# Kernel tuning notes

Measured on AMD Instinct MI355X. Metric: run time of the kernel, lower is better.

## Reference

```python
import jax, jax.numpy as jnp
import numpy as np

B, D_IN, H1, H2, LAT, K = 32768, 512, 256, 128, 64, 2048
BN_EPS = 1e-5
COMMIT = 0.25


def _linear_w(k, i, o):
    # xavier-uniform-ish init
    lim = np.sqrt(6.0 / (i + o)).astype(np.float32)
    return jax.random.uniform(k, (i, o), jnp.float32, -lim, lim)


def _bn_params(keys, n):
    g = jax.random.uniform(keys[0], (n,), jnp.float32, 0.5, 1.5)
    b = 0.1 * jax.random.normal(keys[1], (n,), jnp.float32)
    m = 0.1 * jax.random.normal(keys[2], (n,), jnp.float32)
    v = jax.random.uniform(keys[3], (n,), jnp.float32, 0.5, 1.5)
    return g, b, m, v


def setup_inputs() -> dict:
    key = jax.random.key(0)
    ks = jax.random.split(key, 32)
    inp = {"x": jax.random.normal(ks[0], (B, D_IN), jnp.float32)}
    # encoder: 512 -> 256 -> 128 -> 64
    inp["ew1"], inp["eb1"] = _linear_w(ks[1], D_IN, H1), jnp.zeros((H1,), jnp.float32)
    inp["eg1"], inp["ebt1"], inp["em1"], inp["ev1"] = _bn_params(jax.random.split(ks[2], 4), H1)
    inp["ew2"], inp["eb2"] = _linear_w(ks[3], H1, H2), jnp.zeros((H2,), jnp.float32)
    inp["eg2"], inp["ebt2"], inp["em2"], inp["ev2"] = _bn_params(jax.random.split(ks[4], 4), H2)
    inp["ew3"], inp["eb3"] = _linear_w(ks[5], H2, LAT), jnp.zeros((LAT,), jnp.float32)
    # codebook (num_embeddings, latent_dim)
    inp["codebook"] = _linear_w(ks[6], K, LAT).reshape(K, LAT)
    # decoder: 64 -> 128 -> 256 -> 512
    inp["dw1"], inp["db1"] = _linear_w(ks[7], LAT, H2), jnp.zeros((H2,), jnp.float32)
    inp["dg1"], inp["dbt1"], inp["dm1"], inp["dv1"] = _bn_params(jax.random.split(ks[8], 4), H2)
    inp["dw2"], inp["db2"] = _linear_w(ks[9], H2, H1), jnp.zeros((H1,), jnp.float32)
    inp["dg2"], inp["dbt2"], inp["dm2"], inp["dv2"] = _bn_params(jax.random.split(ks[10], 4), H1)
    inp["dw3"], inp["db3"] = _linear_w(ks[11], H1, D_IN), jnp.zeros((D_IN,), jnp.float32)
    return inp


def _bn(x, g, b, m, v):
    # BatchNorm1d in eval mode: running stats
    return (x - m) * (g * jax.lax.rsqrt(v + BN_EPS)) + b


def reference(x, ew1, eb1, eg1, ebt1, em1, ev1,
              ew2, eb2, eg2, ebt2, em2, ev2,
              ew3, eb3, codebook,
              dw1, db1, dg1, dbt1, dm1, dv1,
              dw2, db2, dg2, dbt2, dm2, dv2,
              dw3, db3):
    # ---- encoder MLP (Dropout is identity in eval) ----
    h = _bn(jax.nn.relu(x @ ew1 + eb1), eg1, ebt1, em1, ev1)
    h = _bn(jax.nn.relu(h @ ew2 + eb2), eg2, ebt2, em2, ev2)
    z_e = h @ ew3 + eb3  # [B, LAT]

    # ---- vector quantization: cdist + argmin + gather ----
    # squared L2 distance (argmin-equivalent to cdist p=2)
    d2 = (jnp.sum(z_e * z_e, axis=1, keepdims=True)
          + jnp.sum(codebook * codebook, axis=1)[None, :]
          - 2.0 * (z_e @ codebook.T))  # [B, K]
    idx = jnp.argmin(d2, axis=-1)  # [B]
    z_q = codebook[idx]  # gather, [B, LAT]

    codebook_loss = jnp.mean((z_q - jax.lax.stop_gradient(z_e)) ** 2)
    commit_loss = jnp.mean((z_e - jax.lax.stop_gradient(z_q)) ** 2)
    vq_loss = codebook_loss + COMMIT * commit_loss

    # straight-through estimator
    z_q = z_e + jax.lax.stop_gradient(z_q - z_e)

    # ---- decoder MLP ----
    h = _bn(jax.nn.relu(z_q @ dw1 + db1), dg1, dbt1, dm1, dv1)
    h = _bn(jax.nn.relu(h @ dw2 + db2), dg2, dbt2, dm2, dv2)
    x_recon = h @ dw3 + db3  # [B, D_IN]

    recon_err = jnp.mean((x_recon - x) ** 2)
    return x_recon, vq_loss, idx, recon_err
```

## Files before the change

### kernel.cpp

```cpp
#include <hip/hip_runtime.h>

#define B_ROWS 32768
#define D_IN   512
#define H1_N   256
#define H2_N   128
#define LAT_N  64
#define K_CB   2048

#define BM 128
#define BN 128
#define BK 32

#define VQ_MARGIN 4.0e-3f

typedef __attribute__((ext_vector_type(8))) short s8v;
typedef __attribute__((ext_vector_type(4))) float f4v;

__device__ inline unsigned short f2bf(float f) {
    union { float f; unsigned u; } v; v.f = f;
    unsigned r = v.u + 0x7fffu + ((v.u >> 16) & 1u);
    return (unsigned short)(r >> 16);
}
__device__ inline float bf2f(unsigned short h) {
    union { unsigned u; float f; } v; v.u = ((unsigned)h) << 16;
    return v.f;
}

#define SWZ(row) ((((row) >> 2) & 7) << 3)

template <int MODE>
__global__ __launch_bounds__(256, 2) void gemm_fused(
    const float* __restrict__ A, const float* __restrict__ W,
    const float* __restrict__ bias,
    const float* __restrict__ bn_g, const float* __restrict__ bn_b,
    const float* __restrict__ bn_m, const float* __restrict__ bn_v,
    float* __restrict__ out,
    const float* __restrict__ xref, float* __restrict__ partials,
    int M, int N)
{
    __shared__ float sA[BK][BM];
    __shared__ float sB[BK][BN];
    const int tid = threadIdx.x;
    const int tr = tid >> 4;
    const int tc = tid & 15;
    const int row0 = blockIdx.x * BM;
    const int n0   = blockIdx.y * BN;

    float acc[8][8];
#pragma unroll
    for (int i = 0; i < 8; ++i)
#pragma unroll
        for (int j = 0; j < 8; ++j) acc[i][j] = 0.f;

    for (int k0 = 0; k0 < M; k0 += BK) {
#pragma unroll
        for (int it = 0; it < 4; ++it) {
            int s = tid + it * 256;
            int m = s >> 3;
            int kq = s & 7;
            float4 v = *reinterpret_cast<const float4*>(
                &A[(size_t)(row0 + m) * M + k0 + kq * 4]);
            int kk = kq * 4;
            sA[kk + 0][m ^ SWZ(kk + 0)] = v.x;
            sA[kk + 1][m ^ SWZ(kk + 1)] = v.y;
            sA[kk + 2][m ^ SWZ(kk + 2)] = v.z;
            sA[kk + 3][m ^ SWZ(kk + 3)] = v.w;
        }
#pragma unroll
        for (int it = 0; it < 4; ++it) {
            int s = tid + it * 256;
            int k = s >> 5;
            int nq = s & 31;
            int n = n0 + nq * 4;
            float4 v = make_float4(0.f, 0.f, 0.f, 0.f);
            if (n < N)
                v = *reinterpret_cast<const float4*>(&W[(size_t)(k0 + k) * N + n]);
            *reinterpret_cast<float4*>(&sB[k][nq * 4]) = v;
        }
        __syncthreads();
#pragma unroll 4
        for (int k = 0; k < BK; ++k) {
            int ac = (tr * 8) ^ SWZ(k);
            float4 a0 = *reinterpret_cast<float4*>(&sA[k][ac]);
            float4 a1 = *reinterpret_cast<float4*>(&sA[k][ac + 4]);
            float4 b0 = *reinterpret_cast<float4*>(&sB[k][tc * 8]);
            float4 b1 = *reinterpret_cast<float4*>(&sB[k][tc * 8 + 4]);
            float a[8] = {a0.x, a0.y, a0.z, a0.w, a1.x, a1.y, a1.z, a1.w};
            float b[8] = {b0.x, b0.y, b0.z, b0.w, b1.x, b1.y, b1.z, b1.w};
#pragma unroll
            for (int i = 0; i < 8; ++i)
#pragma unroll
                for (int j = 0; j < 8; ++j)
                    acc[i][j] = fmaf(a[i], b[j], acc[i][j]);
        }
        __syncthreads();
    }

    const int nb = n0 + tc * 8;
    float sq = 0.f;
    if (nb < N) {
        float bi[8], sc[8], sh[8];
#pragma unroll
        for (int j = 0; j < 8; ++j) {
            int n = nb + j;
            bi[j] = bias[n];
            if (MODE == 0) {
                float s = bn_g[n] * rsqrtf(bn_v[n] + 1e-5f);
                sc[j] = s;
                sh[j] = bn_b[n] - bn_m[n] * s;
            }
        }
#pragma unroll
        for (int i = 0; i < 8; ++i) {
            int row = row0 + tr * 8 + i;
            float o[8];
#pragma unroll
            for (int j = 0; j < 8; ++j) {
                float v = acc[i][j] + bi[j];
                if (MODE == 0) {
                    v = v > 0.f ? v : 0.f;
                    v = v * sc[j] + sh[j];
                }
                o[j] = v;
            }
            if (MODE == 2) {
#pragma unroll
                for (int j = 0; j < 8; ++j) {
                    float d = o[j] - xref[(size_t)row * N + nb + j];
                    sq = fmaf(d, d, sq);
                }
            }
            *reinterpret_cast<float4*>(&out[(size_t)row * N + nb]) =
                make_float4(o[0], o[1], o[2], o[3]);
            *reinterpret_cast<float4*>(&out[(size_t)row * N + nb + 4]) =
                make_float4(o[4], o[5], o[6], o[7]);
        }
    }
    if (MODE == 2) {
        __syncthreads();
        float* red = &sA[0][0];
        red[tid] = sq;
        __syncthreads();
        for (int off = 128; off > 0; off >>= 1) {
            if (tid < off) red[tid] += red[tid + off];
            __syncthreads();
        }
        if (tid == 0) partials[blockIdx.y * gridDim.x + blockIdx.x] = red[0];
    }
}

__global__ __launch_bounds__(256) void vq_prep(
    const float* __restrict__ cb, unsigned short* __restrict__ cb_hi,
    unsigned short* __restrict__ cb_lo, float* __restrict__ cn,
    int* __restrict__ rcnt)
{
    if (blockIdx.x == 0 && threadIdx.x == 0) rcnt[0] = 0;
    int j = blockIdx.x * 256 + threadIdx.x;
    float s = 0.f;
#pragma unroll
    for (int lq = 0; lq < 16; ++lq) {
        float4 v = *reinterpret_cast<const float4*>(&cb[(size_t)j * LAT_N + lq * 4]);
        float e[4] = {v.x, v.y, v.z, v.w};
        ushort4 h, l;
        unsigned short* hp = &h.x;
        unsigned short* lp = &l.x;
#pragma unroll
        for (int t = 0; t < 4; ++t) {
            s = fmaf(e[t], e[t], s);
            unsigned short hb = f2bf(e[t]);
            hp[t] = hb;
            lp[t] = f2bf(e[t] - bf2f(hb));
        }
        *reinterpret_cast<ushort4*>(&cb_hi[(size_t)j * LAT_N + lq * 4]) = h;
        *reinterpret_cast<ushort4*>(&cb_lo[(size_t)j * LAT_N + lq * 4]) = l;
    }
    cn[j] = s;
}

__global__ __launch_bounds__(256) void vq_mfma(
    const float* __restrict__ z, const unsigned short* __restrict__ cb_hi,
    const unsigned short* __restrict__ cb_lo, const float* __restrict__ cnorm,
    float4* __restrict__ cand)
{
    const int lane = threadIdx.x & 63;
    const int wid  = blockIdx.x * 4 + (threadIdx.x >> 6);
    const int rbase = (wid >> 3) * 64;
    const int cblk  = wid & 7;
    const int cbase = cblk * 256;
    const int lr = lane & 15;
    const int lg = lane >> 4;

    s8v a_hi[4][2], a_lo[4][2];
#pragma unroll
    for (int rt = 0; rt < 4; ++rt) {
        int row = rbase + rt * 16 + lr;
#pragma unroll
        for (int ks = 0; ks < 2; ++ks) {
            const float* p = &z[(size_t)row * LAT_N + ks * 32 + lg * 8];
            float4 v0 = *reinterpret_cast<const float4*>(p);
            float4 v1 = *reinterpret_cast<const float4*>(p + 4);
            float vv[8] = {v0.x, v0.y, v0.z, v0.w, v1.x, v1.y, v1.z, v1.w};
#pragma unroll
            for (int jj = 0; jj < 8; ++jj) {
                unsigned short hb = f2bf(vv[jj]);
                a_hi[rt][ks][jj] = (short)hb;
                a_lo[rt][ks][jj] = (short)f2bf(vv[jj] - bf2f(hb));
            }
        }
    }

    float b1[4][4], b2[4][4];
    int j1[4][4];
#pragma unroll
    for (int rt = 0; rt < 4; ++rt)
#pragma unroll
        for (int i = 0; i < 4; ++i) {
            b1[rt][i] = 3.4e38f; b2[rt][i] = 3.4e38f; j1[rt][i] = 0;
        }

    for (int ct = 0; ct < 16; ++ct) {
        int col = cbase + ct * 16 + lr;
        const unsigned short* ph = &cb_hi[(size_t)col * LAT_N + lg * 8];
        const unsigned short* pl = &cb_lo[(size_t)col * LAT_N + lg * 8];
        s8v bh0 = *reinterpret_cast<const s8v*>(ph);
        s8v bh1 = *reinterpret_cast<const s8v*>(ph + 32);
        s8v bl0 = *reinterpret_cast<const s8v*>(pl);
        s8v bl1 = *reinterpret_cast<const s8v*>(pl + 32);
        float cn = cnorm[col];
#pragma unroll
        for (int rt = 0; rt < 4; ++rt) {
            f4v acc = {0.f, 0.f, 0.f, 0.f};
            acc = __builtin_amdgcn_mfma_f32_16x16x32_bf16(a_hi[rt][0], bh0, acc, 0, 0, 0);
            acc = __builtin_amdgcn_mfma_f32_16x16x32_bf16(a_hi[rt][1], bh1, acc, 0, 0, 0);
            acc = __builtin_amdgcn_mfma_f32_16x16x32_bf16(a_lo[rt][0], bh0, acc, 0, 0, 0);
            acc = __builtin_amdgcn_mfma_f32_16x16x32_bf16(a_lo[rt][1], bh1, acc, 0, 0, 0);
            acc = __builtin_amdgcn_mfma_f32_16x16x32_bf16(a_hi[rt][0], bl0, acc, 0, 0, 0);
            acc = __builtin_amdgcn_mfma_f32_16x16x32_bf16(a_hi[rt][1], bl1, acc, 0, 0, 0);
#pragma unroll
            for (int i = 0; i < 4; ++i) {
                float d = fmaf(-2.f, acc[i], cn);
                if (d < b1[rt][i]) {
                    b2[rt][i] = b1[rt][i];
                    b1[rt][i] = d;
                    j1[rt][i] = col;
                } else if (d < b2[rt][i]) {
                    b2[rt][i] = d;
                }
            }
        }
    }

#pragma unroll
    for (int off = 1; off < 16; off <<= 1) {
#pragma unroll
        for (int rt = 0; rt < 4; ++rt)
#pragma unroll
            for (int i = 0; i < 4; ++i) {
                float o1 = __shfl_xor(b1[rt][i], off);
                float o2 = __shfl_xor(b2[rt][i], off);
                int oj = __shfl_xor(j1[rt][i], off);
                float nb2 = fminf(fmaxf(b1[rt][i], o1), fminf(b2[rt][i], o2));
                if (o1 < b1[rt][i] ||
                    (o1 == b1[rt][i] && oj < j1[rt][i])) {
                    b1[rt][i] = o1;
                    j1[rt][i] = oj;
                }
                b2[rt][i] = nb2;
            }
    }
    if (lr == 0) {
#pragma unroll
        for (int rt = 0; rt < 4; ++rt)
#pragma unroll
            for (int i = 0; i < 4; ++i) {
                int row = rbase + rt * 16 + lg * 4 + i;
                cand[(size_t)row * 8 + cblk] = make_float4(
                    b1[rt][i], __int_as_float(j1[rt][i]), b2[rt][i], 0.f);
            }
    }
}

__global__ __launch_bounds__(256) void vq_merge(
    const float4* __restrict__ cand, float* __restrict__ idxf,
    int* __restrict__ rlist, int* __restrict__ rcnt)
{
    int row = blockIdx.x * 256 + threadIdx.x;
    const float4* c = &cand[(size_t)row * 8];
    float4 c0 = c[0];
    float b1 = c0.x, b2 = c0.z;
    int j1 = __float_as_int(c0.y);
#pragma unroll
    for (int t = 1; t < 8; ++t) {
        float4 ct = c[t];
        float o1 = ct.x, o2 = ct.z;
        int oj = __float_as_int(ct.y);
        float nb2 = fminf(fmaxf(b1, o1), fminf(b2, o2));
        if (o1 < b1 || (o1 == b1 && oj < j1)) { b1 = o1; j1 = oj; }
        b2 = nb2;
    }
    idxf[row] = (float)j1;
    if (!(b2 - b1 >= VQ_MARGIN)) {
        int s = atomicAdd(rcnt, 1);
        if (s < B_ROWS) rlist[s] = row;
    }
}

#define RB 8
__global__ __launch_bounds__(256) void vq_repair(
    const int* __restrict__ rcnt, const int* __restrict__ rlist,
    const float* __restrict__ z, const float* __restrict__ cb,
    const float* __restrict__ cn, float* __restrict__ idxf)
{
    __shared__ float sz[RB][LAT_N];
    __shared__ float rv[256];
    __shared__ int ri[256];
    const int tid = threadIdx.x;
    const int count = min(rcnt[0], B_ROWS);
    for (int base = blockIdx.x * RB; base < count; base += gridDim.x * RB) {
        int nr = min(RB, count - base);
        __syncthreads();
        for (int s = tid; s < nr * LAT_N; s += 256) {
            int r = s >> 6, d = s & 63;
            int rr = rlist[base + r];
            rr = ((unsigned)rr < (unsigned)B_ROWS) ? rr : 0;
            sz[r][d] = z[(size_t)rr * LAT_N + d];
        }
        __syncthreads();
        float bv[RB];
        int bj[RB];
#pragma unroll
        for (int r = 0; r < RB; ++r) { bv[r] = 3.4e38f; bj[r] = 0; }
        for (int k = 0; k < K_CB / 256; ++k) {
            int cidx = tid + k * 256;
            float acc[RB];
#pragma unroll
            for (int r = 0; r < RB; ++r) acc[r] = 0.f;
            const float* cp = &cb[(size_t)cidx * LAT_N];
#pragma unroll
            for (int d4 = 0; d4 < 16; ++d4) {
                float4 cv = *reinterpret_cast<const float4*>(cp + d4 * 4);
#pragma unroll
                for (int r = 0; r < RB; ++r) {
                    acc[r] = fmaf(sz[r][d4 * 4 + 0], cv.x, acc[r]);
                    acc[r] = fmaf(sz[r][d4 * 4 + 1], cv.y, acc[r]);
                    acc[r] = fmaf(sz[r][d4 * 4 + 2], cv.z, acc[r]);
                    acc[r] = fmaf(sz[r][d4 * 4 + 3], cv.w, acc[r]);
                }
            }
            float cnv = cn[cidx];
#pragma unroll
            for (int r = 0; r < RB; ++r) {
                float d = fmaf(-2.f, acc[r], cnv);
                if (d < bv[r] || (d == bv[r] && cidx < bj[r])) {
                    bv[r] = d; bj[r] = cidx;
                }
            }
        }
        for (int r = 0; r < RB; ++r) {
            if (r >= nr) break;
            rv[tid] = bv[r];
            ri[tid] = bj[r];
            __syncthreads();
            for (int off = 128; off > 0; off >>= 1) {
                if (tid < off) {
                    float ov = rv[tid + off];
                    int oi = ri[tid + off];
                    if (ov < rv[tid] || (ov == rv[tid] && oi < ri[tid])) {
                        rv[tid] = ov; ri[tid] = oi;
                    }
                }
                __syncthreads();
            }
            if (tid == 0) {
                int rr = rlist[base + r];
                if ((unsigned)rr < (unsigned)B_ROWS)
                    idxf[rr] = (float)ri[0];
            }
            __syncthreads();
        }
    }
}

__global__ __launch_bounds__(256) void vq_zqloss(
    const float* __restrict__ idxf, const float* __restrict__ z,
    const float* __restrict__ cb, float* __restrict__ zq,
    float* __restrict__ partials)
{
    __shared__ float red[256];
    int tid = threadIdx.x;
    int row = blockIdx.x * 256 + tid;
    int bj = (int)idxf[row];
    bj = ((unsigned)bj < (unsigned)K_CB) ? bj : 0;
    float sq = 0.f;
#pragma unroll
    for (int lq = 0; lq < 16; ++lq) {
        float4 cv = *reinterpret_cast<const float4*>(&cb[(size_t)bj * LAT_N + lq * 4]);
        float4 zv = *reinterpret_cast<const float4*>(&z[(size_t)row * LAT_N + lq * 4]);
        *reinterpret_cast<float4*>(&zq[(size_t)row * LAT_N + lq * 4]) = cv;
        float d0 = cv.x - zv.x, d1 = cv.y - zv.y;
        float d2 = cv.z - zv.z, d3 = cv.w - zv.w;
        sq = fmaf(d0, d0, sq); sq = fmaf(d1, d1, sq);
        sq = fmaf(d2, d2, sq); sq = fmaf(d3, d3, sq);
    }
    red[tid] = sq;
    __syncthreads();
    for (int off = 128; off > 0; off >>= 1) {
        if (tid < off) red[tid] += red[tid + off];
        __syncthreads();
    }
    if (tid == 0) partials[blockIdx.x] = red[0];
}

__global__ __launch_bounds__(256) void finalize_kernel(
    const float* __restrict__ vqp, int nvq,
    const float* __restrict__ rep, int nre,
    float* __restrict__ vq_out, float* __restrict__ re_out)
{
    __shared__ float s[256];
    int tid = threadIdx.x;
    float a = 0.f;
    for (int i = tid; i < nvq; i += 256) a += vqp[i];
    s[tid] = a;
    __syncthreads();
    for (int off = 128; off > 0; off >>= 1) {
        if (tid < off) s[tid] += s[tid + off];
        __syncthreads();
    }
    if (tid == 0) *vq_out = 1.25f * s[0] / (float)(B_ROWS * LAT_N);
    __syncthreads();
    float b = 0.f;
    for (int i = tid; i < nre; i += 256) b += rep[i];
    s[tid] = b;
    __syncthreads();
    for (int off = 128; off > 0; off >>= 1) {
        if (tid < off) s[tid] += s[tid + off];
        __syncthreads();
    }
    if (tid == 0) *re_out = s[0] / (float)(B_ROWS * D_IN);
}

extern "C" void kernel_launch(void* const* d_in, const int* in_sizes, int n_in,
                              void* d_out, int out_size, void* d_ws, size_t ws_size,
                              hipStream_t stream)
{
    const float* x    = (const float*)d_in[0];
    const float* ew1  = (const float*)d_in[1];
    const float* eb1  = (const float*)d_in[2];
    const float* eg1  = (const float*)d_in[3];
    const float* ebt1 = (const float*)d_in[4];
    const float* em1  = (const float*)d_in[5];
    const float* ev1  = (const float*)d_in[6];
    const float* ew2  = (const float*)d_in[7];
    const float* eb2  = (const float*)d_in[8];
    const float* eg2  = (const float*)d_in[9];
    const float* ebt2 = (const float*)d_in[10];
    const float* em2  = (const float*)d_in[11];
    const float* ev2  = (const float*)d_in[12];
    const float* ew3  = (const float*)d_in[13];
    const float* eb3  = (const float*)d_in[14];
    const float* cb   = (const float*)d_in[15];
    const float* dw1  = (const float*)d_in[16];
    const float* db1  = (const float*)d_in[17];
    const float* dg1  = (const float*)d_in[18];
    const float* dbt1 = (const float*)d_in[19];
    const float* dm1  = (const float*)d_in[20];
    const float* dv1  = (const float*)d_in[21];
    const float* dw2  = (const float*)d_in[22];
    const float* db2  = (const float*)d_in[23];
    const float* dg2  = (const float*)d_in[24];
    const float* dbt2 = (const float*)d_in[25];
    const float* dm2  = (const float*)d_in[26];
    const float* dv2  = (const float*)d_in[27];
    const float* dw3  = (const float*)d_in[28];
    const float* db3  = (const float*)d_in[29];

    float* outf = (float*)d_out;
    const size_t XR_OFF = 0;
    const size_t VQ_OFF = (size_t)B_ROWS * D_IN;
    const size_t IDX_OFF = VQ_OFF + 1;
    const size_t RE_OFF = IDX_OFF + B_ROWS;

    float* wsf = (float*)d_ws;
    size_t off = 0;
    float* buf256 = wsf + off; off += (size_t)B_ROWS * H1_N;
    float* buf128 = wsf + off; off += (size_t)B_ROWS * H2_N;
    float* zbuf   = wsf + off; off += (size_t)B_ROWS * LAT_N;
    float* zqbuf  = wsf + off; off += (size_t)B_ROWS * LAT_N;
    float* cnbuf  = wsf + off; off += K_CB;
    float* vqp    = wsf + off; off += 128;
    float* rep    = wsf + off; off += 1024;
    unsigned short* cbhi = (unsigned short*)(wsf + off); off += K_CB * LAT_N / 2;
    unsigned short* cblo = (unsigned short*)(wsf + off); off += K_CB * LAT_N / 2;
    float4* candb = (float4*)(wsf + off); off += (size_t)B_ROWS * 8 * 4;
    int* rcnt  = (int*)(wsf + off); off += 16;
    int* rlist = (int*)(wsf + off); off += B_ROWS;

    dim3 blk(256);
    const int GX = B_ROWS / BM;

    vq_prep<<<dim3(K_CB / 256), blk, 0, stream>>>(cb, cbhi, cblo, cnbuf, rcnt);

    gemm_fused<0><<<dim3(GX, H1_N / BN), blk, 0, stream>>>(
        x, ew1, eb1, eg1, ebt1, em1, ev1, buf256, nullptr, nullptr, D_IN, H1_N);
    gemm_fused<0><<<dim3(GX, 1), blk, 0, stream>>>(
        buf256, ew2, eb2, eg2, ebt2, em2, ev2, buf128, nullptr, nullptr, H1_N, H2_N);
    gemm_fused<1><<<dim3(GX, 1), blk, 0, stream>>>(
        buf128, ew3, eb3, nullptr, nullptr, nullptr, nullptr, zbuf, nullptr, nullptr,
        H2_N, LAT_N);

    vq_mfma<<<dim3(1024), blk, 0, stream>>>(zbuf, cbhi, cblo, cnbuf, candb);
    vq_merge<<<dim3(B_ROWS / 256), blk, 0, stream>>>(
        candb, outf + IDX_OFF, rlist, rcnt);
    vq_repair<<<dim3(128), blk, 0, stream>>>(
        rcnt, rlist, zbuf, cb, cnbuf, outf + IDX_OFF);
    vq_zqloss<<<dim3(B_ROWS / 256), blk, 0, stream>>>(
        outf + IDX_OFF, zbuf, cb, zqbuf, vqp);

    gemm_fused<0><<<dim3(GX, 1), blk, 0, stream>>>(
        zqbuf, dw1, db1, dg1, dbt1, dm1, dv1, buf128, nullptr, nullptr, LAT_N, H2_N);
    gemm_fused<0><<<dim3(GX, H1_N / BN), blk, 0, stream>>>(
        buf128, dw2, db2, dg2, dbt2, dm2, dv2, buf256, nullptr, nullptr, H2_N, H1_N);
    gemm_fused<2><<<dim3(GX, D_IN / BN), blk, 0, stream>>>(
        buf256, dw3, db3, nullptr, nullptr, nullptr, nullptr, outf + XR_OFF,
        x, rep, H1_N, D_IN);

    finalize_kernel<<<dim3(1), blk, 0, stream>>>(
        vqp, 128, rep, 1024, outf + VQ_OFF, outf + RE_OFF);
}
```

Before: 479.7 us.

## Run decoder GEMMs on MFMA with split-bf16 three-product emulation

Replaces the three FP32 SIMT decoder GEMMs with a new MFMA kernel. Activations are split on the fly into bf16 hi/lo parts, and weights are pre-split and transposed by a new prep kernel; three bf16 MFMAs approximate FP32 accuracy. Operands are loaded straight from global memory without LDS tiling, and the recon-error reduction moves into the new kernel. The aim is to remove the FP32 FMA compute bound, at the cost of uncoalesced per-element output stores and some precision loss.

```diff
diff --git a/kernel.cpp b/kernel.cpp
--- a/kernel.cpp
+++ b/kernel.cpp
@@ -97,7 +97,6 @@
     }
 
     const int nb = n0 + tc * 8;
-    float sq = 0.f;
     if (nb < N) {
         float bi[8], sc[8], sh[8];
 #pragma unroll
@@ -123,29 +122,133 @@
                 }
                 o[j] = v;
             }
-            if (MODE == 2) {
-#pragma unroll
-                for (int j = 0; j < 8; ++j) {
-                    float d = o[j] - xref[(size_t)row * N + nb + j];
-                    sq = fmaf(d, d, sq);
-                }
-            }
             *reinterpret_cast<float4*>(&out[(size_t)row * N + nb]) =
                 make_float4(o[0], o[1], o[2], o[3]);
             *reinterpret_cast<float4*>(&out[(size_t)row * N + nb + 4]) =
                 make_float4(o[4], o[5], o[6], o[7]);
         }
     }
+}
+
+__global__ __launch_bounds__(256) void wprep(
+    const float* __restrict__ w, unsigned short* __restrict__ w_hi,
+    unsigned short* __restrict__ w_lo, int K, int N)
+{
+    int idx = blockIdx.x * 256 + threadIdx.x;
+    if (idx >= N * K) return;
+    int n = idx / K, k = idx - n * K;
+    float f = w[(size_t)k * N + n];
+    unsigned u = __float_as_uint(f);
+    float lo = f - __uint_as_float(u & 0xffff0000u);
+    w_hi[idx] = (unsigned short)(u >> 16);
+    w_lo[idx] = (unsigned short)(__float_as_uint(lo) >> 16);
+}
+
+template <int MODE, int K>
+__global__ __launch_bounds__(256, 2) void mfma_gemm(
+    const float* __restrict__ A,
+    const unsigned short* __restrict__ w_hi,
+    const unsigned short* __restrict__ w_lo,
+    const float* __restrict__ bias,
+    const float* __restrict__ bn_g, const float* __restrict__ bn_b,
+    const float* __restrict__ bn_m, const float* __restrict__ bn_v,
+    float* __restrict__ out,
+    const float* __restrict__ xref, float* __restrict__ partials, int N)
+{
+    const int lane = threadIdx.x & 63;
+    const int wv = threadIdx.x >> 6;
+    const int wr = wv >> 1, wc = wv & 1;
+    const int rbase = blockIdx.x * 128 + wr * 64;
+    const int cbase = blockIdx.y * 128 + wc * 64;
+    const int lr = lane & 15, lg = lane >> 4;
+
+    f4v acc[4][4];
+#pragma unroll
+    for (int rt = 0; rt < 4; ++rt)
+#pragma unroll
+        for (int ct = 0; ct < 4; ++ct)
+            acc[rt][ct] = (f4v){0.f, 0.f, 0.f, 0.f};
+
+#pragma unroll
+    for (int ks = 0; ks < K / 32; ++ks) {
+        s8v ah[4], al[4], bh[4], bl[4];
+#pragma unroll
+        for (int rt = 0; rt < 4; ++rt) {
+            const float* p =
+                &A[(size_t)(rbase + rt * 16 + lr) * K + ks * 32 + lg * 8];
+            float4 v0 = *reinterpret_cast<const float4*>(p);
+            float4 v1 = *reinterpret_cast<const float4*>(p + 4);
+            float fv[8] = {v0.x, v0.y, v0.z, v0.w, v1.x, v1.y, v1.z, v1.w};
+            unsigned uu[8], ll[8];
+#pragma unroll
+            for (int j = 0; j < 8; ++j) {
+                uu[j] = __float_as_uint(fv[j]);
+                float lo = fv[j] - __uint_as_float(uu[j] & 0xffff0000u);
+                ll[j] = __float_as_uint(lo);
+            }
+            union { s8v v; unsigned w[4]; } H, L;
+#pragma unroll
+            for (int m = 0; m < 4; ++m) {
+                H.w[m] = __builtin_amdgcn_perm(uu[2 * m + 1], uu[2 * m], 0x07060302u);
+                L.w[m] = __builtin_amdgcn_perm(ll[2 * m + 1], ll[2 * m], 0x07060302u);
+            }
+            ah[rt] = H.v;
+            al[rt] = L.v;
+        }
+#pragma unroll
+        for (int ct = 0; ct < 4; ++ct) {
+            size_t off = (size_t)(cbase + ct * 16 + lr) * K + ks * 32 + lg * 8;
+            bh[ct] = *reinterpret_cast<const s8v*>(&w_hi[off]);
+            bl[ct] = *reinterpret_cast<const s8v*>(&w_lo[off]);
+        }
+#pragma unroll
+        for (int rt = 0; rt < 4; ++rt)
+#pragma unroll
+            for (int ct = 0; ct < 4; ++ct) {
+                acc[rt][ct] = __builtin_amdgcn_mfma_f32_16x16x32_bf16(
+                    ah[rt], bh[ct], acc[rt][ct], 0, 0, 0);
+                acc[rt][ct] = __builtin_amdgcn_mfma_f32_16x16x32_bf16(
+                    al[rt], bh[ct], acc[rt][ct], 0, 0, 0);
+                acc[rt][ct] = __builtin_amdgcn_mfma_f32_16x16x32_bf16(
+                    ah[rt], bl[ct], acc[rt][ct], 0, 0, 0);
+            }
+    }
+
+    float sq = 0.f;
+#pragma unroll
+    for (int ct = 0; ct < 4; ++ct) {
+        int col = cbase + ct * 16 + lr;
+        float bi = bias[col];
+        float sc = 0.f, sh = 0.f;
+        if (MODE == 0) {
+            float s = bn_g[col] * rsqrtf(bn_v[col] + 1e-5f);
+            sc = s;
+            sh = bn_b[col] - bn_m[col] * s;
+        }
+#pragma unroll
+        for (int rt = 0; rt < 4; ++rt)
+#pragma unroll
+            for (int i = 0; i < 4; ++i) {
+                int row = rbase + rt * 16 + lg * 4 + i;
+                float v = acc[rt][ct][i] + bi;
+                if (MODE == 0) v = fmaxf(v, 0.f) * sc + sh;
+                if (MODE == 2) {
+                    float d = v - xref[(size_t)row * N + col];
+                    sq = fmaf(d, d, sq);
+                }
+                out[(size_t)row * N + col] = v;
+            }
+    }
     if (MODE == 2) {
-        __syncthreads();
-        float* red = &sA[0][0];
-        red[tid] = sq;
+        __shared__ float red[256];
+        red[threadIdx.x] = sq;
         __syncthreads();
         for (int off = 128; off > 0; off >>= 1) {
-            if (tid < off) red[tid] += red[tid + off];
+            if (threadIdx.x < off) red[threadIdx.x] += red[threadIdx.x + off];
             __syncthreads();
         }
-        if (tid == 0) partials[blockIdx.y * gridDim.x + blockIdx.x] = red[0];
+        if (threadIdx.x == 0)
+            partials[blockIdx.y * gridDim.x + blockIdx.x] = red[0];
     }
 }
 
@@ -494,11 +597,21 @@
     float4* candb = (float4*)(wsf + off); off += (size_t)B_ROWS * 8 * 4;
     int* rcnt  = (int*)(wsf + off); off += 16;
     int* rlist = (int*)(wsf + off); off += B_ROWS;
+    unsigned short* w1hi = (unsigned short*)(wsf + off); off += (H2_N * LAT_N) / 2;
+    unsigned short* w1lo = (unsigned short*)(wsf + off); off += (H2_N * LAT_N) / 2;
+    unsigned short* w2hi = (unsigned short*)(wsf + off); off += (H1_N * H2_N) / 2;
+    unsigned short* w2lo = (unsigned short*)(wsf + off); off += (H1_N * H2_N) / 2;
+    unsigned short* w3hi = (unsigned short*)(wsf + off); off += (D_IN * H1_N) / 2;
+    unsigned short* w3lo = (unsigned short*)(wsf + off); off += (D_IN * H1_N) / 2;
 
     dim3 blk(256);
     const int GX = B_ROWS / BM;
+    const int GXM = B_ROWS / 128;
 
     vq_prep<<<dim3(K_CB / 256), blk, 0, stream>>>(cb, cbhi, cblo, cnbuf, rcnt);
+    wprep<<<dim3((LAT_N * H2_N + 255) / 256), blk, 0, stream>>>(dw1, w1hi, w1lo, LAT_N, H2_N);
+    wprep<<<dim3((H2_N * H1_N + 255) / 256), blk, 0, stream>>>(dw2, w2hi, w2lo, H2_N, H1_N);
+    wprep<<<dim3((H1_N * D_IN + 255) / 256), blk, 0, stream>>>(dw3, w3hi, w3lo, H1_N, D_IN);
 
     gemm_fused<0><<<dim3(GX, H1_N / BN), blk, 0, stream>>>(
         x, ew1, eb1, eg1, ebt1, em1, ev1, buf256, nullptr, nullptr, D_IN, H1_N);
@@ -516,13 +629,13 @@
     vq_zqloss<<<dim3(B_ROWS / 256), blk, 0, stream>>>(
         outf + IDX_OFF, zbuf, cb, zqbuf, vqp);
 
-    gemm_fused<0><<<dim3(GX, 1), blk, 0, stream>>>(
-        zqbuf, dw1, db1, dg1, dbt1, dm1, dv1, buf128, nullptr, nullptr, LAT_N, H2_N);
-    gemm_fused<0><<<dim3(GX, H1_N / BN), blk, 0, stream>>>(
-        buf128, dw2, db2, dg2, dbt2, dm2, dv2, buf256, nullptr, nullptr, H2_N, H1_N);
-    gemm_fused<2><<<dim3(GX, D_IN / BN), blk, 0, stream>>>(
-        buf256, dw3, db3, nullptr, nullptr, nullptr, nullptr, outf + XR_OFF,
-        x, rep, H1_N, D_IN);
+    mfma_gemm<0, LAT_N><<<dim3(GXM, H2_N / 128), blk, 0, stream>>>(
+        zqbuf, w1hi, w1lo, db1, dg1, dbt1, dm1, dv1, buf128, nullptr, nullptr, H2_N);
+    mfma_gemm<0, H2_N><<<dim3(GXM, H1_N / 128), blk, 0, stream>>>(
+        buf128, w2hi, w2lo, db2, dg2, dbt2, dm2, dv2, buf256, nullptr, nullptr, H1_N);
+    mfma_gemm<2, H1_N><<<dim3(GXM, D_IN / 128), blk, 0, stream>>>(
+        buf256, w3hi, w3lo, db3, nullptr, nullptr, nullptr, nullptr,
+        outf + XR_OFF, x, rep, D_IN);
 
     finalize_kernel<<<dim3(1), blk, 0, stream>>>(
         vqp, 128, rep, 1024, outf + VQ_OFF, outf + RE_OFF);
```

New measurement: 439.5 us. -8.4%, faster.
